# Kernel optimization log

Measured on AMD Instinct MI355X. Metric: run time of the kernel, lower is better.

## Reference

```python
import jax, jax.numpy as jnp
import numpy as np

POOL = (7, 7)


def crop_and_resize(fmap, boxes, box_idx, ph, pw):
    """tf.image.crop_and_resize (bilinear) for normalized boxes (y1,x1,y2,x2).
    fmap: [B,H,W,C], boxes: [N,4], box_idx: [N] int32 -> [N,ph,pw,C]."""
    H, W = fmap.shape[1], fmap.shape[2]
    dt = fmap.dtype
    y1, x1, y2, x2 = boxes[:, 0], boxes[:, 1], boxes[:, 2], boxes[:, 3]
    ty = jnp.arange(ph, dtype=dt) / (ph - 1)
    tx = jnp.arange(pw, dtype=dt) / (pw - 1)
    ys = (y1[:, None] + ty[None, :] * (y2 - y1)[:, None]) * (H - 1)  # [N,ph]
    xs = (x1[:, None] + tx[None, :] * (x2 - x1)[:, None]) * (W - 1)  # [N,pw]
    y0f = jnp.clip(jnp.floor(ys), 0.0, H - 1)
    x0f = jnp.clip(jnp.floor(xs), 0.0, W - 1)
    y0 = y0f.astype(jnp.int32)
    x0 = x0f.astype(jnp.int32)
    y1i = jnp.minimum(y0 + 1, H - 1)
    x1i = jnp.minimum(x0 + 1, W - 1)
    wy = (ys - y0f)[:, :, None, None]  # [N,ph,1,1]
    wx = (xs - x0f)[:, None, :, None]  # [N,1,pw,1]
    b = box_idx[:, None, None]
    v00 = fmap[b, y0[:, :, None], x0[:, None, :]]  # [N,ph,pw,C]
    v01 = fmap[b, y0[:, :, None], x1i[:, None, :]]
    v10 = fmap[b, y1i[:, :, None], x0[:, None, :]]
    v11 = fmap[b, y1i[:, :, None], x1i[:, None, :]]
    top = v00 + (v01 - v00) * wx
    bot = v10 + (v11 - v10) * wx
    return top + (bot - top) * wy


def setup_inputs() -> dict:
    key = jax.random.key(0)
    k1, k2, k3, k4, kp2, kp3, kp4, kp5 = jax.random.split(key, 8)
    B, N, C = 1, 1000, 256
    y1 = jax.random.uniform(k1, (B, N)) * 0.7
    x1 = jax.random.uniform(k2, (B, N)) * 0.7
    h = jax.random.uniform(k3, (B, N)) * 0.4 + 0.01
    w = jax.random.uniform(k4, (B, N)) * 0.4 + 0.01
    ROIboxes = jnp.stack([y1, x1, jnp.minimum(y1 + h, 1.0), jnp.minimum(x1 + w, 1.0)], axis=-1)
    meta = np.zeros((B, 93), np.float32)
    meta[:, 4:7] = [1024.0, 1024.0, 3.0]  # image_shape
    return {
        "ROIboxes": ROIboxes.astype(jnp.float32),
        "image_meta": jnp.asarray(meta),
        "P2": jax.random.normal(kp2, (B, 256, 256, C), jnp.float32),
        "P3": jax.random.normal(kp3, (B, 128, 128, C), jnp.float32),
        "P4": jax.random.normal(kp4, (B, 64, 64, C), jnp.float32),
        "P5": jax.random.normal(kp5, (B, 32, 32, C), jnp.float32),
    }


def reference(ROIboxes, image_meta, P2, P3, P4, P5):
    feature_maps = [P2, P3, P4, P5]
    B, N = ROIboxes.shape[0], ROIboxes.shape[1]
    boxes = jax.lax.stop_gradient(ROIboxes.reshape(-1, 4))  # [B*N,4]
    box_idx = jnp.repeat(jnp.arange(B, dtype=jnp.int32), N)
    image_shape = image_meta[0, 4:7]
    image_area = image_shape[0] * image_shape[1]
    h = boxes[:, 2] - boxes[:, 0]
    w = boxes[:, 3] - boxes[:, 1]
    roi_level = jnp.log2(jnp.sqrt(h * w) / (224.0 / jnp.sqrt(image_area)))
    roi_level = jnp.clip(4 + jnp.round(roi_level).astype(jnp.int32), 2, 5)  # [B*N]
    ph, pw = POOL
    C = P2.shape[-1]
    pooled = jnp.zeros((B * N, ph, pw, C), P2.dtype)
    for i, level in enumerate(range(2, 6)):
        p = crop_and_resize(feature_maps[i], boxes, box_idx, ph, pw)
        mask = (roi_level == level)[:, None, None, None]
        pooled = pooled + jnp.where(mask, p, 0.0)
    # Original gathers per-level then sorts back to original ROI order; the
    # masked-sum above produces the same per-ROI result in original order.
    return pooled[None]  # [1, B*N, ph, pw, C]
```

## Files before the change

kernel.cpp:

```cpp
#include <hip/hip_runtime.h>
#include <hip/hip_bf16.h>
#include <math.h>


#define CCH 256
#define PH 7
#define PW 7

__global__ __launch_bounds__(256) void PyramidROIAlign_kernel(
    const float* __restrict__ boxes,
    const float* __restrict__ meta,
    const float* __restrict__ P2,
    const float* __restrict__ P3,
    const float* __restrict__ P4,
    const float* __restrict__ P5,
    float* __restrict__ out,
    int total_boxes,
    int n_per_batch)
{
    int wid  = (blockIdx.x * blockDim.x + threadIdx.x) >> 6;
    int lane = threadIdx.x & 63;
    if (wid >= total_boxes * PH) return;
    wid = __builtin_amdgcn_readfirstlane(wid);

    int n  = wid / PH;
    int py = wid - n * PH;

    float y1 = boxes[n * 4 + 0];
    float x1 = boxes[n * 4 + 1];
    float y2 = boxes[n * 4 + 2];
    float x2 = boxes[n * 4 + 3];

    float area  = meta[4] * meta[5];
    float scale = 224.0f / sqrtf(area);
    float lvlf  = log2f(sqrtf((y2 - y1) * (x2 - x1)) / scale);
    int level = 4 + (int)rintf(lvlf);
    level = min(max(level, 2), 5);

    const float* fmap;
    int H;
    switch (level) {
        case 2:  fmap = P2; H = 256; break;
        case 3:  fmap = P3; H = 128; break;
        case 4:  fmap = P4; H = 64;  break;
        default: fmap = P5; H = 32;  break;
    }
    int W = H;
    int b = n / n_per_batch;
    fmap += (size_t)b * H * W * CCH;

    float ty  = (float)py / (float)(PH - 1);
    float ys  = (y1 + ty * (y2 - y1)) * (float)(H - 1);
    float y0f = fminf(fmaxf(floorf(ys), 0.0f), (float)(H - 1));
    int   y0  = (int)y0f;
    int   y1r = min(y0 + 1, H - 1);
    float wy  = ys - y0f;

    const float* row0 = fmap + (size_t)y0  * W * CCH;
    const float* row1 = fmap + (size_t)y1r * W * CCH;

    int c = lane << 2;
    float* optr = out + ((size_t)wid * PW) * CCH + c;

    #pragma unroll
    for (int px = 0; px < PW; ++px) {
        float tx  = (float)px / (float)(PW - 1);
        float xs  = (x1 + tx * (x2 - x1)) * (float)(W - 1);
        float x0f = fminf(fmaxf(floorf(xs), 0.0f), (float)(W - 1));
        int   x0  = (int)x0f;
        int   x1r = min(x0 + 1, W - 1);
        float wx  = xs - x0f;

        int o0 = x0  * CCH + c;
        int o1 = x1r * CCH + c;
        float4 v00 = *(const float4*)(row0 + o0);
        float4 v01 = *(const float4*)(row0 + o1);
        float4 v10 = *(const float4*)(row1 + o0);
        float4 v11 = *(const float4*)(row1 + o1);

        float4 o;
        float top, bot;
        top = v00.x + (v01.x - v00.x) * wx;
        bot = v10.x + (v11.x - v10.x) * wx;
        o.x = top + (bot - top) * wy;
        top = v00.y + (v01.y - v00.y) * wx;
        bot = v10.y + (v11.y - v10.y) * wx;
        o.y = top + (bot - top) * wy;
        top = v00.z + (v01.z - v00.z) * wx;
        bot = v10.z + (v11.z - v10.z) * wx;
        o.z = top + (bot - top) * wy;
        top = v00.w + (v01.w - v00.w) * wx;
        bot = v10.w + (v11.w - v10.w) * wx;
        o.w = top + (bot - top) * wy;

        *((float4*)(optr + px * CCH)) = o;
    }
}

extern "C" void kernel_launch(void* const* d_in, const int* in_sizes, int n_in,
                              void* d_out, int out_size, void* d_ws, size_t ws_size,
                              hipStream_t stream) {
    const float* boxes = (const float*)d_in[0];
    const float* meta  = (const float*)d_in[1];
    const float* P2    = (const float*)d_in[2];
    const float* P3    = (const float*)d_in[3];
    const float* P4    = (const float*)d_in[4];
    const float* P5    = (const float*)d_in[5];
    float* out = (float*)d_out;

    int total_boxes = in_sizes[0] / 4;
    int B = in_sizes[1] / 93;
    if (B < 1) B = 1;
    int n_per_batch = total_boxes / B;

    long total_threads = (long)total_boxes * PH * 64;
    int threads = 256;
    int blocks = (int)((total_threads + threads - 1) / threads);

    PyramidROIAlign_kernel<<<blocks, threads, 0, stream>>>(
        boxes, meta, P2, P3, P4, P5, out, total_boxes, n_per_batch);
}
```

Before: 29.76 us.

## Remap blocks across XCDs and software-prefetch next column's bilinear taps

```diff
diff --git a/kernel.cpp b/kernel.cpp
--- a/kernel.cpp
+++ b/kernel.cpp
@@ -6,8 +6,9 @@
 #define CCH 256
 #define PH 7
 #define PW 7
+#define NXCD 8
 
-__global__ __launch_bounds__(256) void PyramidROIAlign_kernel(
+__global__ __launch_bounds__(256, 4) void PyramidROIAlign_kernel(
     const float* __restrict__ boxes,
     const float* __restrict__ meta,
     const float* __restrict__ P2,
@@ -18,7 +19,13 @@
     int total_boxes,
     int n_per_batch)
 {
-    int wid  = (blockIdx.x * blockDim.x + threadIdx.x) >> 6;
+    int nwg = gridDim.x;
+    int q = nwg / NXCD, r = nwg % NXCD;
+    int xcd = blockIdx.x % NXCD;
+    int off = blockIdx.x / NXCD;
+    int bid = (xcd < r ? xcd * (q + 1) : r * (q + 1) + (xcd - r) * q) + off;
+
+    int wid  = bid * (256 / 64) + (threadIdx.x >> 6);
     int lane = threadIdx.x & 63;
     if (wid >= total_boxes * PH) return;
     wid = __builtin_amdgcn_readfirstlane(wid);
@@ -56,44 +63,59 @@
     int   y1r = min(y0 + 1, H - 1);
     float wy  = ys - y0f;
 
-    const float* row0 = fmap + (size_t)y0  * W * CCH;
-    const float* row1 = fmap + (size_t)y1r * W * CCH;
+    int c = lane << 2;
+    const float* row0 = fmap + (size_t)y0  * W * CCH + c;
+    const float* row1 = fmap + (size_t)y1r * W * CCH + c;
 
-    int c = lane << 2;
-    float* optr = out + ((size_t)wid * PW) * CCH + c;
-
+    int   o0[PW], o1[PW];
+    float wxv[PW];
     #pragma unroll
     for (int px = 0; px < PW; ++px) {
         float tx  = (float)px / (float)(PW - 1);
         float xs  = (x1 + tx * (x2 - x1)) * (float)(W - 1);
         float x0f = fminf(fmaxf(floorf(xs), 0.0f), (float)(W - 1));
         int   x0  = (int)x0f;
-        int   x1r = min(x0 + 1, W - 1);
-        float wx  = xs - x0f;
+        int   x1c = min(x0 + 1, W - 1);
+        wxv[px] = xs - x0f;
+        o0[px] = x0  * CCH;
+        o1[px] = x1c * CCH;
+    }
 
-        int o0 = x0  * CCH + c;
-        int o1 = x1r * CCH + c;
-        float4 v00 = *(const float4*)(row0 + o0);
-        float4 v01 = *(const float4*)(row0 + o1);
-        float4 v10 = *(const float4*)(row1 + o0);
-        float4 v11 = *(const float4*)(row1 + o1);
+    float* optr = out + ((size_t)wid * PW) * CCH + c;
 
+    float4 a00 = *(const float4*)(row0 + o0[0]);
+    float4 a01 = *(const float4*)(row0 + o1[0]);
+    float4 a10 = *(const float4*)(row1 + o0[0]);
+    float4 a11 = *(const float4*)(row1 + o1[0]);
+
+    #pragma unroll
+    for (int px = 0; px < PW; ++px) {
+        float4 b00, b01, b10, b11;
+        if (px + 1 < PW) {
+            b00 = *(const float4*)(row0 + o0[px + 1]);
+            b01 = *(const float4*)(row0 + o1[px + 1]);
+            b10 = *(const float4*)(row1 + o0[px + 1]);
+            b11 = *(const float4*)(row1 + o1[px + 1]);
+        }
+        float wx = wxv[px];
         float4 o;
         float top, bot;
-        top = v00.x + (v01.x - v00.x) * wx;
-        bot = v10.x + (v11.x - v10.x) * wx;
+        top = a00.x + (a01.x - a00.x) * wx;
+        bot = a10.x + (a11.x - a10.x) * wx;
         o.x = top + (bot - top) * wy;
-        top = v00.y + (v01.y - v00.y) * wx;
-        bot = v10.y + (v11.y - v10.y) * wx;
+        top = a00.y + (a01.y - a00.y) * wx;
+        bot = a10.y + (a11.y - a10.y) * wx;
         o.y = top + (bot - top) * wy;
-        top = v00.z + (v01.z - v00.z) * wx;
-        bot = v10.z + (v11.z - v10.z) * wx;
+        top = a00.z + (a01.z - a00.z) * wx;
+        bot = a10.z + (a11.z - a10.z) * wx;
         o.z = top + (bot - top) * wy;
-        top = v00.w + (v01.w - v00.w) * wx;
-        bot = v10.w + (v11.w - v10.w) * wx;
+        top = a00.w + (a01.w - a00.w) * wx;
+        bot = a10.w + (a11.w - a10.w) * wx;
         o.w = top + (bot - top) * wy;
 
         *((float4*)(optr + px * CCH)) = o;
+
+        a00 = b00; a01 = b01; a10 = b10; a11 = b11;
     }
 }
 
@@ -113,10 +135,9 @@
     if (B < 1) B = 1;
     int n_per_batch = total_boxes / B;
 
-    long total_threads = (long)total_boxes * PH * 64;
-    int threads = 256;
-    int blocks = (int)((total_threads + threads - 1) / threads);
+    long total_waves = (long)total_boxes * PH;
+    int blocks = (int)((total_waves + 3) / 4);
 
-    PyramidROIAlign_kernel<<<blocks, threads, 0, stream>>>(
+    PyramidROIAlign_kernel<<<blocks, 256, 0, stream>>>(
         boxes, meta, P2, P3, P4, P5, out, total_boxes, n_per_batch);
 }
```

After: 29.42 us. No clear change (-1.1%).

## Sort ROIs by level and spatial bin, remap blocks per XCD for cache locality

Applied to the files above, without the earlier changes.

```diff
diff --git a/kernel.cpp b/kernel.cpp
--- a/kernel.cpp
+++ b/kernel.cpp
@@ -6,25 +6,79 @@
 #define CCH 256
 #define PH 7
 #define PW 7
+#define NXCD 8
 
-__global__ __launch_bounds__(256) void PyramidROIAlign_kernel(
+typedef float nat_float4 __attribute__((ext_vector_type(4)));
+
+__global__ __launch_bounds__(256) void sort_boxes_kernel(
+    const float* __restrict__ boxes, const float* __restrict__ meta,
+    int* __restrict__ perm, int total_boxes)
+{
+    __shared__ int hist[256];
+    __shared__ int base[256];
+    int tid = threadIdx.x;
+    hist[tid] = 0;
+    __syncthreads();
+
+    float area  = meta[4] * meta[5];
+    float scale = 224.0f / sqrtf(area);
+
+    for (int i = tid; i < total_boxes; i += 256) {
+        float y1 = boxes[i * 4 + 0], x1 = boxes[i * 4 + 1];
+        float y2 = boxes[i * 4 + 2], x2 = boxes[i * 4 + 3];
+        int lvl = 4 + (int)rintf(log2f(sqrtf((y2 - y1) * (x2 - x1)) / scale));
+        lvl = min(max(lvl, 2), 5);
+        int yb = min(7, max(0, (int)((y1 + y2) * 4.0f)));
+        int xb = min(7, max(0, (int)((x1 + x2) * 4.0f)));
+        int key = ((lvl - 2) << 6) | (yb << 3) | xb;
+        atomicAdd(&hist[key], 1);
+    }
+    __syncthreads();
+    if (tid == 0) {
+        int acc = 0;
+        for (int k = 0; k < 256; ++k) { base[k] = acc; acc += hist[k]; }
+    }
+    __syncthreads();
+    for (int i = tid; i < total_boxes; i += 256) {
+        float y1 = boxes[i * 4 + 0], x1 = boxes[i * 4 + 1];
+        float y2 = boxes[i * 4 + 2], x2 = boxes[i * 4 + 3];
+        int lvl = 4 + (int)rintf(log2f(sqrtf((y2 - y1) * (x2 - x1)) / scale));
+        lvl = min(max(lvl, 2), 5);
+        int yb = min(7, max(0, (int)((y1 + y2) * 4.0f)));
+        int xb = min(7, max(0, (int)((x1 + x2) * 4.0f)));
+        int key = ((lvl - 2) << 6) | (yb << 3) | xb;
+        int pos = atomicAdd(&base[key], 1);
+        perm[pos] = i;
+    }
+}
+
+__global__ __launch_bounds__(256, 4) void PyramidROIAlign_kernel(
     const float* __restrict__ boxes,
     const float* __restrict__ meta,
     const float* __restrict__ P2,
     const float* __restrict__ P3,
     const float* __restrict__ P4,
     const float* __restrict__ P5,
+    const int*   __restrict__ perm,
     float* __restrict__ out,
     int total_boxes,
     int n_per_batch)
 {
-    int wid  = (blockIdx.x * blockDim.x + threadIdx.x) >> 6;
+    int nwg = gridDim.x;
+    int q = nwg / NXCD, r = nwg % NXCD;
+    int xcd = blockIdx.x % NXCD;
+    int off = blockIdx.x / NXCD;
+    int bid = (xcd < r ? xcd * (q + 1) : r * (q + 1) + (xcd - r) * q) + off;
+
+    int wid  = bid * 4 + (threadIdx.x >> 6);
     int lane = threadIdx.x & 63;
     if (wid >= total_boxes * PH) return;
     wid = __builtin_amdgcn_readfirstlane(wid);
 
-    int n  = wid / PH;
-    int py = wid - n * PH;
+    int spos = wid / PH;
+    int py   = wid - spos * PH;
+    int n    = perm[spos];
+    n = __builtin_amdgcn_readfirstlane(n);
 
     float y1 = boxes[n * 4 + 0];
     float x1 = boxes[n * 4 + 1];
@@ -56,11 +110,11 @@
     int   y1r = min(y0 + 1, H - 1);
     float wy  = ys - y0f;
 
-    const float* row0 = fmap + (size_t)y0  * W * CCH;
-    const float* row1 = fmap + (size_t)y1r * W * CCH;
+    int c = lane << 2;
+    const float* row0 = fmap + (size_t)y0  * W * CCH + c;
+    const float* row1 = fmap + (size_t)y1r * W * CCH + c;
 
-    int c = lane << 2;
-    float* optr = out + ((size_t)wid * PW) * CCH + c;
+    float* optr = out + ((size_t)n * (PH * PW) + py * PW) * CCH + c;
 
     #pragma unroll
     for (int px = 0; px < PW; ++px) {
@@ -68,17 +122,17 @@
         float xs  = (x1 + tx * (x2 - x1)) * (float)(W - 1);
         float x0f = fminf(fmaxf(floorf(xs), 0.0f), (float)(W - 1));
         int   x0  = (int)x0f;
-        int   x1r = min(x0 + 1, W - 1);
+        int   x1c = min(x0 + 1, W - 1);
         float wx  = xs - x0f;
 
-        int o0 = x0  * CCH + c;
-        int o1 = x1r * CCH + c;
+        int o0 = x0  * CCH;
+        int o1 = x1c * CCH;
         float4 v00 = *(const float4*)(row0 + o0);
         float4 v01 = *(const float4*)(row0 + o1);
         float4 v10 = *(const float4*)(row1 + o0);
         float4 v11 = *(const float4*)(row1 + o1);
 
-        float4 o;
+        nat_float4 o;
         float top, bot;
         top = v00.x + (v01.x - v00.x) * wx;
         bot = v10.x + (v11.x - v10.x) * wx;
@@ -93,7 +147,7 @@
         bot = v10.w + (v11.w - v10.w) * wx;
         o.w = top + (bot - top) * wy;
 
-        *((float4*)(optr + px * CCH)) = o;
+        __builtin_nontemporal_store(o, (nat_float4*)(optr + px * CCH));
     }
 }
 
@@ -107,16 +161,18 @@
     const float* P4    = (const float*)d_in[4];
     const float* P5    = (const float*)d_in[5];
     float* out = (float*)d_out;
+    int*   perm = (int*)d_ws;
 
     int total_boxes = in_sizes[0] / 4;
     int B = in_sizes[1] / 93;
     if (B < 1) B = 1;
     int n_per_batch = total_boxes / B;
 
-    long total_threads = (long)total_boxes * PH * 64;
-    int threads = 256;
-    int blocks = (int)((total_threads + threads - 1) / threads);
+    sort_boxes_kernel<<<1, 256, 0, stream>>>(boxes, meta, perm, total_boxes);
 
-    PyramidROIAlign_kernel<<<blocks, threads, 0, stream>>>(
-        boxes, meta, P2, P3, P4, P5, out, total_boxes, n_per_batch);
+    long total_waves = (long)total_boxes * PH;
+    int blocks = (int)((total_waves + 3) / 4);
+
+    PyramidROIAlign_kernel<<<blocks, 256, 0, stream>>>(
+        boxes, meta, P2, P3, P4, P5, perm, out, total_boxes, n_per_batch);
 }
```

New measurement: 29.52 us. Within noise of the previous version (-0.8%).
